# Performance work log

Measured on AMD Instinct MI355X. Metric: run time of the kernel, lower is better.

## Reference

```python
import jax, jax.numpy as jnp
import numpy as np

B, S, A = 64, 512, 20
V, E, H, L = 130, 64, 64, 2


def _lstm_step(x, layers):
    # One timestep through L stacked LSTM layers with zero initial state
    # (the original passes state=None on every call; eval mode, no dropout).
    h_list, c_list = [], []
    inp = x
    for (Wih, Whh, bih, bhh) in layers:
        g = inp @ Wih.T + bih + bhh  # h=0, c=0 => Whh term vanishes
        i, f, gg, o = jnp.split(g, 4, axis=-1)  # PyTorch gate order i,f,g,o
        c = jax.nn.sigmoid(i) * jnp.tanh(gg)
        h = jax.nn.sigmoid(o) * jnp.tanh(c)
        h_list.append(h); c_list.append(c)
        inp = h
    return inp, jnp.stack(h_list), jnp.stack(c_list)  # [B,H], [L,B,H], [L,B,H]


def _forward(emb, Wih0, Whh0, bih0, bhh0, Wih1, Whh1, bih1, bhh1,
             Whw, Whb, Wcw, Wcb, vw, vb, decw, decb, inputs, lengths):
    Ls = np.asarray(lengths)
    steps = int(Ls.max())
    batch = inputs.shape[0]
    layers = [(Wih0, Whh0, bih0, bhh0), (Wih1, Whh1, bih1, bhh1)]
    # embeddings = embedding(inputs.permute(1,0)); loop uses rows 0 and 1 only
    x0 = emb[inputs[:, 0]]
    x1 = emb[inputs[:, 1]]  # BUG in original: every step i>=1 reuses embeddings[1]
    out0, h0, c0 = _lstm_step(x0, layers)
    out1, h1, c1 = _lstm_step(x1, layers)
    # Replicate torch cat + .view() memory reinterpretation exactly.
    outputs = jnp.concatenate(
        [out0[None], jnp.broadcast_to(out1[None], (steps - 1, batch, H))], 0
    ).reshape(batch, steps, H)
    h_steps = jnp.concatenate(
        [h0, jnp.broadcast_to(h1[None], (steps - 1, L, batch, H)).reshape((steps - 1) * L, batch, H)], 0
    ).reshape(batch, steps, L * H)
    c_steps = jnp.concatenate(
        [c0, jnp.broadcast_to(c1[None], (steps - 1, L, batch, H)).reshape((steps - 1) * L, batch, H)], 0
    ).reshape(batch, steps, L * H)
    Wh = h_steps @ Whw.T + Whb  # [B,S,H]
    Wc = c_steps @ Wcw.T + Wcb  # [B,S,H]
    # Sliding window: Att[b,i,j] = Wh[b, i - A + j] where valid, else 0.
    idx = jnp.arange(steps)[:, None] + jnp.arange(A)[None, :] - A  # [S,A]
    valid = idx >= 0
    win = jnp.where(valid[None, :, :, None], Wh[:, jnp.clip(idx, 0), :], 0.0)  # [B,S,A,H]
    # In the original, Wh_att aliases Att, so the in-place += Wc hits both.
    att = win + Wc[:, :, None, :]
    att_w = jnp.tan(att) @ vw.T + vb  # torch.tan, not tanh
    # Mask loop: iteration i=0 sets Att_weight[:, :, 0:A] = -1e9, i.e. ALL of it.
    att_w = jnp.full_like(att_w, -1e9)
    sw = jax.nn.softmax(att_w, axis=2)  # exactly uniform 1/A
    attn = jnp.sum(sw * att, axis=2)  # [B,S,H]
    concat_h = jnp.concatenate([attn, outputs], axis=2)  # [B,S,2H]
    outs = concat_h @ decw.T + decb  # [B,S,V]
    # flatten_padded_sequences: concat of outs[b, :L[b]-1] over batch (static lengths)
    bi, ti = np.nonzero(np.arange(steps)[None, :] < (Ls[:, None] - 1))
    return outs[bi, ti].reshape(-1, V)


def setup_inputs() -> dict:
    key = jax.random.key(0)
    ks = jax.random.split(key, 20)
    f32 = jnp.float32
    d = {
        "emb": jax.random.normal(ks[0], (V, E), f32) * 0.05,
        "Wih0": jax.random.normal(ks[1], (4 * H, E), f32) * 0.05,
        "Whh0": jax.random.normal(ks[2], (4 * H, H), f32) * 0.05,
        "bih0": jax.random.normal(ks[3], (4 * H,), f32) * 0.05,
        "bhh0": jax.random.normal(ks[4], (4 * H,), f32) * 0.05,
        "Wih1": jax.random.normal(ks[5], (4 * H, H), f32) * 0.05,
        "Whh1": jax.random.normal(ks[6], (4 * H, H), f32) * 0.05,
        "bih1": jax.random.normal(ks[7], (4 * H,), f32) * 0.05,
        "bhh1": jax.random.normal(ks[8], (4 * H,), f32) * 0.05,
        "Whw": jax.random.normal(ks[9], (H, L * H), f32) * 0.05,
        "Whb": jax.random.normal(ks[10], (H,), f32) * 0.05,
        "Wcw": jax.random.normal(ks[11], (H, L * H), f32) * 0.05,
        "Wcb": jax.random.normal(ks[12], (H,), f32) * 0.05,
        "vw": jax.random.normal(ks[13], (1, H), f32) * 0.05,
        "vb": jax.random.normal(ks[14], (1,), f32) * 0.05,
        "decw": jax.random.normal(ks[15], (V, 2 * H), f32) * 0.05,
        "decb": jax.random.normal(ks[16], (V,), f32) * 0.05,
        "inputs": jax.random.randint(ks[17], (B, S), 0, V, dtype=jnp.int32),
        "lengths": jnp.full((B,), S, dtype=jnp.int32),
    }
    return d


def reference(emb, Wih0, Whh0, bih0, bhh0, Wih1, Whh1, bih1, bhh1,
              Whw, Whb, Wcw, Wcb, vw, vb, decw, decb, inputs, lengths):
    return _forward(emb, Wih0, Whh0, bih0, bhh0, Wih1, Whh1, bih1, bhh1,
                    Whw, Whb, Wcw, Wcb, vw, vb, decw, decb, inputs, lengths)
```

## Files before the change

### kernel.cpp

```cpp
#include <hip/hip_runtime.h>
#include <math.h>


#define STEPS 512
#define VOCAB 130

__device__ __forceinline__ float sigf(float x) { return 1.0f / (1.0f + expf(-x)); }

__global__ __launch_bounds__(256) void k_lstm(
    const float* __restrict__ emb,
    const float* __restrict__ Wih0, const float* __restrict__ bih0, const float* __restrict__ bhh0,
    const float* __restrict__ Wih1, const float* __restrict__ bih1, const float* __restrict__ bhh1,
    const int* __restrict__ inputs,
    float* __restrict__ hst, float* __restrict__ cst)
{
    __shared__ float x[64];
    __shared__ float g[256];
    __shared__ float hmid[64];
    const int b   = blockIdx.x & 63;
    const int tok = blockIdx.x >> 6;
    const int tid = threadIdx.x;
    if (tid < 64) {
        int token = inputs[b * STEPS + tok];
        x[tid] = emb[token * 64 + tid];
    }
    __syncthreads();
    float acc = bih0[tid] + bhh0[tid];
    {
        const float* w = Wih0 + tid * 64;
        #pragma unroll
        for (int e = 0; e < 64; ++e) acc = fmaf(x[e], w[e], acc);
    }
    g[tid] = acc;
    __syncthreads();
    if (tid < 64) {
        float i = g[tid], gg = g[128 + tid], o = g[192 + tid];
        float c = sigf(i) * tanhf(gg);
        float h = sigf(o) * tanhf(c);
        hst[((tok * 2 + 0) * 64 + b) * 64 + tid] = h;
        cst[((tok * 2 + 0) * 64 + b) * 64 + tid] = c;
        hmid[tid] = h;
    }
    __syncthreads();
    acc = bih1[tid] + bhh1[tid];
    {
        const float* w = Wih1 + tid * 64;
        #pragma unroll
        for (int e = 0; e < 64; ++e) acc = fmaf(hmid[e], w[e], acc);
    }
    g[tid] = acc;
    __syncthreads();
    if (tid < 64) {
        float i = g[tid], gg = g[128 + tid], o = g[192 + tid];
        float c = sigf(i) * tanhf(gg);
        float h = sigf(o) * tanhf(c);
        hst[((tok * 2 + 1) * 64 + b) * 64 + tid] = h;
        cst[((tok * 2 + 1) * 64 + b) * 64 + tid] = c;
    }
}

__global__ __launch_bounds__(128) void k_whwc(
    const float* __restrict__ Whw, const float* __restrict__ Whb,
    const float* __restrict__ Wcw, const float* __restrict__ Wcb,
    const float* __restrict__ hst, const float* __restrict__ cst,
    float* __restrict__ Wh, float* __restrict__ Wc)
{
    __shared__ float hrow[128], crow[128];
    const int cls = blockIdx.x >> 9;
    const int t2  = blockIdx.x & 511;
    const int j   = threadIdx.x;
    const int r = (cls == 0) ? (t2 >> 5) : (16 + (t2 >> 5));
    int tok, lay;
    if (r == 0)      { tok = 0; lay = 0; }
    else if (r == 1) { tok = 0; lay = 1; }
    else             { tok = 1; lay = (r & 1); }
    const int bb  = 2 * (t2 & 31) + (j >> 6);
    const int src = ((tok * 2 + lay) * 64 + bb) * 64 + (j & 63);
    hrow[j] = hst[src];
    crow[j] = cst[src];
    __syncthreads();
    if (j < 64) {
        float acc = Whb[j];
        const float* w = Whw + j * 128;
        #pragma unroll
        for (int k = 0; k < 128; ++k) acc = fmaf(hrow[k], w[k], acc);
        Wh[(cls * 512 + t2) * 64 + j] = acc;
    } else {
        const int jj = j - 64;
        float acc = Wcb[jj];
        const float* w = Wcw + jj * 128;
        #pragma unroll
        for (int k = 0; k < 128; ++k) acc = fmaf(crow[k], w[k], acc);
        Wc[(cls * 512 + t2) * 64 + jj] = acc;
    }
}

__global__ __launch_bounds__(256) void k_dec_bcast(
    const float* __restrict__ Wh, const float* __restrict__ Wc,
    const float* __restrict__ hst,
    const float* __restrict__ decw, const float* __restrict__ decb,
    float* __restrict__ out)
{
    __shared__ float cc[128];
    __shared__ float row[VOCAB];
    const int t2  = blockIdx.x;
    const int cls = blockIdx.y;
    const int tid = threadIdx.x;
    if (tid < 64) {
        float s = 0.0f;
        const int k0 = (t2 >= 20) ? (t2 - 20) : 0;
        for (int k = k0; k < t2; ++k) s += Wh[(cls * 512 + k) * 64 + tid];
        cc[tid] = Wc[(cls * 512 + t2) * 64 + tid] + 0.05f * s;
    } else if (tid < 128) {
        const int tok = (cls == 0 && t2 < 64) ? 0 : 1;
        cc[tid] = hst[((tok * 2 + 1) * 64 + (t2 & 63)) * 64 + (tid - 64)];
    }
    __syncthreads();
    if (tid < VOCAB) {
        float acc = decb[tid];
        const float* w = decw + tid * 128;
        #pragma unroll
        for (int k = 0; k < 128; ++k) acc = fmaf(cc[k], w[k], acc);
        row[tid] = acc;
    }
    __syncthreads();
    if (cls == 0) {
        if (tid < VOCAB) out[t2 * VOCAB + tid] = row[tid];
    } else {
        float v = (tid < VOCAB) ? row[tid] : 0.0f;
        for (int b = 1; b < 64; ++b)
            if (tid < VOCAB) out[(b * 511 + t2) * VOCAB + tid] = v;
    }
}

extern "C" void kernel_launch(void* const* d_in, const int* in_sizes, int n_in,
                              void* d_out, int out_size, void* d_ws, size_t ws_size,
                              hipStream_t stream)
{
    const float* emb  = (const float*)d_in[0];
    const float* Wih0 = (const float*)d_in[1];
    const float* bih0 = (const float*)d_in[3];
    const float* bhh0 = (const float*)d_in[4];
    const float* Wih1 = (const float*)d_in[5];
    const float* bih1 = (const float*)d_in[7];
    const float* bhh1 = (const float*)d_in[8];
    const float* Whw  = (const float*)d_in[9];
    const float* Whb  = (const float*)d_in[10];
    const float* Wcw  = (const float*)d_in[11];
    const float* Wcb  = (const float*)d_in[12];
    const float* decw = (const float*)d_in[15];
    const float* decb = (const float*)d_in[16];
    const int* inputs = (const int*)d_in[17];

    float* ws  = (float*)d_ws;
    float* hst = ws;
    float* cst = hst + 16384;
    float* Wh  = cst + 16384;
    float* Wc  = Wh + 65536;

    hipLaunchKernelGGL(k_lstm, dim3(128), dim3(256), 0, stream,
                       emb, Wih0, bih0, bhh0, Wih1, bih1, bhh1, inputs, hst, cst);
    hipLaunchKernelGGL(k_whwc, dim3(1024), dim3(128), 0, stream,
                       Whw, Whb, Wcw, Wcb, hst, cst, Wh, Wc);
    hipLaunchKernelGGL(k_dec_bcast, dim3(511, 2), dim3(256), 0, stream,
                       Wh, Wc, hst, decw, decb, (float*)d_out);
}
```

Measured before the change: 123.6 us.

## Fuse LSTM recompute into projection and decoder kernels; vectorize broadcast stores

Removes the standalone LSTM kernel by recomputing the two-layer LSTM cell inside each block of the Wh/Wc projection kernel and the decoder kernel, so hst/cst no longer go through global memory and one launch disappears. The decoder's broadcast of rows across 63 batches now uses float2 stores spread over all threads instead of 130-thread scalar loops. The price is redundant LSTM arithmetic and weight reads in every block (over a thousand blocks in total), which adds compute and latency per block.

```diff
diff --git a/kernel.cpp b/kernel.cpp
--- a/kernel.cpp
+++ b/kernel.cpp
@@ -7,78 +7,89 @@
 
 __device__ __forceinline__ float sigf(float x) { return 1.0f / (1.0f + expf(-x)); }
 
-__global__ __launch_bounds__(256) void k_lstm(
+__global__ __launch_bounds__(128) void k_whwc_fused(
     const float* __restrict__ emb,
     const float* __restrict__ Wih0, const float* __restrict__ bih0, const float* __restrict__ bhh0,
     const float* __restrict__ Wih1, const float* __restrict__ bih1, const float* __restrict__ bhh1,
     const int* __restrict__ inputs,
-    float* __restrict__ hst, float* __restrict__ cst)
-{
-    __shared__ float x[64];
-    __shared__ float g[256];
-    __shared__ float hmid[64];
-    const int b   = blockIdx.x & 63;
-    const int tok = blockIdx.x >> 6;
-    const int tid = threadIdx.x;
-    if (tid < 64) {
-        int token = inputs[b * STEPS + tok];
-        x[tid] = emb[token * 64 + tid];
-    }
-    __syncthreads();
-    float acc = bih0[tid] + bhh0[tid];
-    {
-        const float* w = Wih0 + tid * 64;
-        #pragma unroll
-        for (int e = 0; e < 64; ++e) acc = fmaf(x[e], w[e], acc);
-    }
-    g[tid] = acc;
-    __syncthreads();
-    if (tid < 64) {
-        float i = g[tid], gg = g[128 + tid], o = g[192 + tid];
-        float c = sigf(i) * tanhf(gg);
-        float h = sigf(o) * tanhf(c);
-        hst[((tok * 2 + 0) * 64 + b) * 64 + tid] = h;
-        cst[((tok * 2 + 0) * 64 + b) * 64 + tid] = c;
-        hmid[tid] = h;
-    }
-    __syncthreads();
-    acc = bih1[tid] + bhh1[tid];
-    {
-        const float* w = Wih1 + tid * 64;
-        #pragma unroll
-        for (int e = 0; e < 64; ++e) acc = fmaf(hmid[e], w[e], acc);
-    }
-    g[tid] = acc;
-    __syncthreads();
-    if (tid < 64) {
-        float i = g[tid], gg = g[128 + tid], o = g[192 + tid];
-        float c = sigf(i) * tanhf(gg);
-        float h = sigf(o) * tanhf(c);
-        hst[((tok * 2 + 1) * 64 + b) * 64 + tid] = h;
-        cst[((tok * 2 + 1) * 64 + b) * 64 + tid] = c;
-    }
-}
-
-__global__ __launch_bounds__(128) void k_whwc(
     const float* __restrict__ Whw, const float* __restrict__ Whb,
     const float* __restrict__ Wcw, const float* __restrict__ Wcb,
-    const float* __restrict__ hst, const float* __restrict__ cst,
     float* __restrict__ Wh, float* __restrict__ Wc)
 {
+    __shared__ float x[2][64];
+    __shared__ float g[2][256];
+    __shared__ float hmid[2][64];
     __shared__ float hrow[128], crow[128];
-    const int cls = blockIdx.x >> 9;
-    const int t2  = blockIdx.x & 511;
+    const int t2  = blockIdx.x;
+    const int cls = blockIdx.y;
     const int j   = threadIdx.x;
+
     const int r = (cls == 0) ? (t2 >> 5) : (16 + (t2 >> 5));
     int tok, lay;
     if (r == 0)      { tok = 0; lay = 0; }
     else if (r == 1) { tok = 0; lay = 1; }
     else             { tok = 1; lay = (r & 1); }
-    const int bb  = 2 * (t2 & 31) + (j >> 6);
-    const int src = ((tok * 2 + lay) * 64 + bb) * 64 + (j & 63);
-    hrow[j] = hst[src];
-    crow[j] = cst[src];
-    __syncthreads();
+    const int bb0 = 2 * (t2 & 31);
+
+    {
+        const int v = j >> 6, e = j & 63;
+        const int token = inputs[(bb0 + v) * STEPS + tok];
+        x[v][e] = emb[token * 64 + e];
+    }
+    __syncthreads();
+
+    #pragma unroll
+    for (int v = 0; v < 2; ++v) {
+        float a0 = bih0[j] + bhh0[j];
+        float a1 = bih0[j + 128] + bhh0[j + 128];
+        const float* w0 = Wih0 + j * 64;
+        const float* w1 = Wih0 + (j + 128) * 64;
+        #pragma unroll
+        for (int e = 0; e < 64; ++e) {
+            const float xv = x[v][e];
+            a0 = fmaf(xv, w0[e], a0);
+            a1 = fmaf(xv, w1[e], a1);
+        }
+        g[v][j] = a0; g[v][j + 128] = a1;
+    }
+    __syncthreads();
+    {
+        const int v = j >> 6, e = j & 63;
+        const float i  = g[v][e], gg = g[v][128 + e], o = g[v][192 + e];
+        const float c  = sigf(i) * tanhf(gg);
+        const float h  = sigf(o) * tanhf(c);
+        hmid[v][e] = h;
+        if (lay == 0) { hrow[j] = h; crow[j] = c; }
+    }
+    __syncthreads();
+    if (lay == 1) {
+        #pragma unroll
+        for (int v = 0; v < 2; ++v) {
+            float a0 = bih1[j] + bhh1[j];
+            float a1 = bih1[j + 128] + bhh1[j + 128];
+            const float* w0 = Wih1 + j * 64;
+            const float* w1 = Wih1 + (j + 128) * 64;
+            #pragma unroll
+            for (int e = 0; e < 64; ++e) {
+                const float hv = hmid[v][e];
+                a0 = fmaf(hv, w0[e], a0);
+                a1 = fmaf(hv, w1[e], a1);
+            }
+            g[v][j] = a0; g[v][j + 128] = a1;
+        }
+        __syncthreads();
+        {
+            const int v = j >> 6, e = j & 63;
+            const float i  = g[v][e], gg = g[v][128 + e], o = g[v][192 + e];
+            const float c  = sigf(i) * tanhf(gg);
+            const float h  = sigf(o) * tanhf(c);
+            hrow[j] = h; crow[j] = c;
+        }
+        __syncthreads();
+    } else {
+        __syncthreads();
+    }
+
     if (j < 64) {
         float acc = Whb[j];
         const float* w = Whw + j * 128;
@@ -96,24 +107,63 @@
 }
 
 __global__ __launch_bounds__(256) void k_dec_bcast(
+    const float* __restrict__ emb,
+    const float* __restrict__ Wih0, const float* __restrict__ bih0, const float* __restrict__ bhh0,
+    const float* __restrict__ Wih1, const float* __restrict__ bih1, const float* __restrict__ bhh1,
+    const int* __restrict__ inputs,
     const float* __restrict__ Wh, const float* __restrict__ Wc,
-    const float* __restrict__ hst,
     const float* __restrict__ decw, const float* __restrict__ decb,
     float* __restrict__ out)
 {
+    __shared__ float x[64];
+    __shared__ float g[256];
+    __shared__ float hmid[64];
     __shared__ float cc[128];
     __shared__ float row[VOCAB];
     const int t2  = blockIdx.x;
     const int cls = blockIdx.y;
     const int tid = threadIdx.x;
+
+    const int tok = (cls == 0 && t2 < 64) ? 0 : 1;
+    const int b   = t2 & 63;
+
     if (tid < 64) {
+        const int token = inputs[b * STEPS + tok];
+        x[tid] = emb[token * 64 + tid];
+    }
+    __syncthreads();
+    {
+        float a = bih0[tid] + bhh0[tid];
+        const float* w = Wih0 + tid * 64;
+        #pragma unroll
+        for (int e = 0; e < 64; ++e) a = fmaf(x[e], w[e], a);
+        g[tid] = a;
+    }
+    __syncthreads();
+    if (tid < 64) {
+        const float i = g[tid], gg = g[128 + tid], o = g[192 + tid];
+        const float c = sigf(i) * tanhf(gg);
+        hmid[tid] = sigf(o) * tanhf(c);
+    }
+    __syncthreads();
+    {
+        float a = bih1[tid] + bhh1[tid];
+        const float* w = Wih1 + tid * 64;
+        #pragma unroll
+        for (int e = 0; e < 64; ++e) a = fmaf(hmid[e], w[e], a);
+        g[tid] = a;
+    }
+    __syncthreads();
+    if (tid < 64) {
+        const float i = g[tid], gg = g[128 + tid], o = g[192 + tid];
+        const float c = sigf(i) * tanhf(gg);
+        cc[64 + tid] = sigf(o) * tanhf(c);
+    } else if (tid < 128) {
+        const int e = tid - 64;
         float s = 0.0f;
         const int k0 = (t2 >= 20) ? (t2 - 20) : 0;
-        for (int k = k0; k < t2; ++k) s += Wh[(cls * 512 + k) * 64 + tid];
-        cc[tid] = Wc[(cls * 512 + t2) * 64 + tid] + 0.05f * s;
-    } else if (tid < 128) {
-        const int tok = (cls == 0 && t2 < 64) ? 0 : 1;
-        cc[tid] = hst[((tok * 2 + 1) * 64 + (t2 & 63)) * 64 + (tid - 64)];
+        for (int k = k0; k < t2; ++k) s += Wh[(cls * 512 + k) * 64 + e];
+        cc[e] = Wc[(cls * 512 + t2) * 64 + e] + 0.05f * s;
     }
     __syncthreads();
     if (tid < VOCAB) {
@@ -127,9 +177,12 @@
     if (cls == 0) {
         if (tid < VOCAB) out[t2 * VOCAB + tid] = row[tid];
     } else {
-        float v = (tid < VOCAB) ? row[tid] : 0.0f;
-        for (int b = 1; b < 64; ++b)
-            if (tid < VOCAB) out[(b * 511 + t2) * VOCAB + tid] = v;
+        for (int i = tid; i < 4095; i += 256) {
+            const int b2 = 1 + i / 65;
+            const int wi = i - (i / 65) * 65;
+            float2 v = make_float2(row[2 * wi], row[2 * wi + 1]);
+            *reinterpret_cast<float2*>(out + (size_t)(b2 * 511 + t2) * VOCAB + 2 * wi) = v;
+        }
     }
 }
 
@@ -152,16 +205,14 @@
     const float* decb = (const float*)d_in[16];
     const int* inputs = (const int*)d_in[17];
 
-    float* ws  = (float*)d_ws;
-    float* hst = ws;
-    float* cst = hst + 16384;
-    float* Wh  = cst + 16384;
-    float* Wc  = Wh + 65536;
-
-    hipLaunchKernelGGL(k_lstm, dim3(128), dim3(256), 0, stream,
-                       emb, Wih0, bih0, bhh0, Wih1, bih1, bhh1, inputs, hst, cst);
-    hipLaunchKernelGGL(k_whwc, dim3(1024), dim3(128), 0, stream,
-                       Whw, Whb, Wcw, Wcb, hst, cst, Wh, Wc);
+    float* ws = (float*)d_ws;
+    float* Wh = ws;
+    float* Wc = Wh + 65536;
+
+    hipLaunchKernelGGL(k_whwc_fused, dim3(512, 2), dim3(128), 0, stream,
+                       emb, Wih0, bih0, bhh0, Wih1, bih1, bhh1, inputs,
+                       Whw, Whb, Wcw, Wcb, Wh, Wc);
     hipLaunchKernelGGL(k_dec_bcast, dim3(511, 2), dim3(256), 0, stream,
-                       Wh, Wc, hst, decw, decb, (float*)d_out);
+                       emb, Wih0, bih0, bhh0, Wih1, bih1, bhh1, inputs,
+                       Wh, Wc, decw, decb, (float*)d_out);
 }
```

New measurement: 190.0 us. 53.6% more time.
